# Kernel tuning notes

Hardware: AMD Instinct MI355X
Metric: run time of the kernel (lower is better)

Reference implementation:

```python
import jax, jax.numpy as jnp
import numpy as np

K = 8               # top-k frequencies
PRED_LEN = 96       # prediction_length
LOW_FREQ = 1        # low_frequency cutoff (drops DC)


def setup_inputs() -> dict:
    key = jax.random.key(0)
    x = jax.random.normal(key, (32, 2048, 64), dtype=jnp.float32)
    return {"x": x}


def reference(x):
    b, t, d = x.shape
    x_freq = jnp.fft.rfft(x, axis=1)                 # (b, t//2+1, d) complex
    freqs = jnp.fft.rfftfreq(t).astype(x.dtype)
    if t % 2 == 0:
        x_freq = x_freq[:, LOW_FREQ:-1]              # drop DC and Nyquist
        f = freqs[LOW_FREQ:-1]
    else:
        x_freq = x_freq[:, LOW_FREQ:]
        f = freqs[LOW_FREQ:]

    # top-k over frequency dim (axis=1), independently per (b, d)
    mag = jnp.abs(x_freq)                            # (b, F, d)
    _, idx = jax.lax.top_k(jnp.moveaxis(mag, 1, 2), K)  # (b, d, K), sorted desc
    idx = jnp.moveaxis(idx, 1, 2)                    # (b, K, d)
    x_k = jnp.take_along_axis(x_freq, idx, axis=1)   # (b, K, d) complex
    f_k = f[idx]                                     # (b, K, d)

    # extrapolate: add conjugate (negative) frequencies, then cos-sum
    x2 = jnp.concatenate([x_k, jnp.conj(x_k)], axis=1)  # (b, 2K, d)
    f2 = jnp.concatenate([f_k, -f_k], axis=1)           # (b, 2K, d)
    t_val = jnp.arange(t + PRED_LEN, dtype=x.dtype)     # (T,)
    amp = jnp.abs(x2) / t                               # (b, 2K, d)
    phase = jnp.angle(x2)                               # (b, 2K, d)
    # (b, 2K, T, d) broadcast intermediate, reduced over freq axis
    x_time = amp[:, :, None, :] * jnp.cos(
        2.0 * np.float32(np.pi) * f2[:, :, None, :] * t_val[None, None, :, None]
        + phase[:, :, None, :]
    )
    return x_time.sum(axis=1)                        # (b, t+PRED_LEN, d)
```

## Files before the change

### kernel.cpp

```cpp
#include <hip/hip_runtime.h>
#include <math.h>

#define BB 32
#define TT 2048
#define DD 64
#define PRED 96
#define TP (TT + PRED)
#define KTOP 8
#define NCAND 12
#define NSIG (BB * DD)
#define MARGIN 2e-4f
#define PI_D 3.14159265358979323846

__device__ __forceinline__ int physIdx(int idx) { return idx ^ ((idx >> 5) & 31); }

__device__ __forceinline__ int posOf(int k) {
    return ((k & 7) << 8) | (((k >> 3) & 7) << 5) | (((k >> 6) & 7) << 2) | (k >> 9);
}

__device__ __forceinline__ float2 cadd(float2 a, float2 b) { return make_float2(a.x + b.x, a.y + b.y); }
__device__ __forceinline__ float2 csub(float2 a, float2 b) { return make_float2(a.x - b.x, a.y - b.y); }
__device__ __forceinline__ float2 cmulni(float2 a) { return make_float2(a.y, -a.x); }
__device__ __forceinline__ float2 cmulpi(float2 a) { return make_float2(-a.y, a.x); }
__device__ __forceinline__ float2 cw8(float2 a) {
    const float s = 0.70710678118654752f;
    return make_float2(s * (a.x + a.y), s * (a.y - a.x));
}
__device__ __forceinline__ float2 cw83(float2 a) {
    const float s = 0.70710678118654752f;
    return make_float2(s * (a.y - a.x), -s * (a.x + a.y));
}
__device__ __forceinline__ float2 ctw(float2 a, int m) {
    const float rev = (float)m * (1.0f / 2048.0f);
    const float c = __builtin_amdgcn_cosf(rev);
    const float s = __builtin_amdgcn_sinf(rev);
    return make_float2(a.x * c + a.y * s, a.y * c - a.x * s);
}

__device__ __forceinline__ void radix8(float2* r) {
    float2 E0, E1, E2, E3, O0, O1, O2, O3;
    {
        float2 s0 = cadd(r[0], r[4]), s1 = csub(r[0], r[4]);
        float2 s2 = cadd(r[2], r[6]), s3 = csub(r[2], r[6]);
        E0 = cadd(s0, s2); E2 = csub(s0, s2);
        E1 = cadd(s1, cmulni(s3)); E3 = cadd(s1, cmulpi(s3));
    }
    {
        float2 s0 = cadd(r[1], r[5]), s1 = csub(r[1], r[5]);
        float2 s2 = cadd(r[3], r[7]), s3 = csub(r[3], r[7]);
        O0 = cadd(s0, s2); O2 = csub(s0, s2);
        O1 = cadd(s1, cmulni(s3)); O3 = cadd(s1, cmulpi(s3));
    }
    const float2 w1 = cw8(O1), w2 = cmulni(O2), w3 = cw83(O3);
    r[0] = cadd(E0, O0); r[4] = csub(E0, O0);
    r[1] = cadd(E1, w1); r[5] = csub(E1, w1);
    r[2] = cadd(E2, w2); r[6] = csub(E2, w2);
    r[3] = cadd(E3, w3); r[7] = csub(E3, w3);
}

__global__ __launch_bounds__(256) void fft_topk_kernel(const float* __restrict__ x,
                                                       int* __restrict__ idxw,
                                                       float* __restrict__ rew,
                                                       float* __restrict__ imw) {
    __shared__ float2 Z[TT];
    __shared__ unsigned long long keys[TT];
    __shared__ int    candS[2][NCAND];
    __shared__ int    flagS[2];
    __shared__ double resR[2][NCAND], resI[2][NCAND], resM[2][NCAND];
    __shared__ double2 wA[32];
    __shared__ double2 wB[64];

    const int i    = blockIdx.x;
    const int xcd  = i & 7;
    const int slot = i >> 3;
    const int b    = xcd * 4 + (slot >> 5);
    const int dp   = slot & 31;
    const int t    = threadIdx.x;

    const float2* xv = (const float2*)x;
    const size_t base = (size_t)b * TT * (DD / 2) + dp;
    float2 r[8];
    #pragma unroll
    for (int q = 0; q < 8; ++q) r[q] = xv[base + (size_t)(t + 256 * q) * (DD / 2)];

    radix8(r);
    #pragma unroll
    for (int p = 1; p < 8; ++p) r[p] = ctw(r[p], (p * t) & (TT - 1));
    #pragma unroll
    for (int p = 0; p < 8; ++p) Z[physIdx(t + (p << 8))] = r[p];
    __syncthreads();

    const int S2 = (t >> 5) << 8, j2 = t & 31;
    #pragma unroll
    for (int p = 0; p < 8; ++p) r[p] = Z[physIdx(S2 + j2 + (p << 5))];
    radix8(r);
    #pragma unroll
    for (int p = 1; p < 8; ++p) r[p] = ctw(r[p], (8 * p * j2) & (TT - 1));
    #pragma unroll
    for (int p = 0; p < 8; ++p) Z[physIdx(S2 + j2 + (p << 5))] = r[p];
    __syncthreads();

    const int S3 = (t >> 2) << 5, j3 = t & 3;
    #pragma unroll
    for (int p = 0; p < 8; ++p) r[p] = Z[physIdx(S3 + j3 + (p << 2))];
    radix8(r);
    #pragma unroll
    for (int p = 1; p < 8; ++p) r[p] = ctw(r[p], (64 * p * j3) & (TT - 1));
    #pragma unroll
    for (int p = 0; p < 8; ++p) Z[physIdx(S3 + j3 + (p << 2))] = r[p];
    __syncthreads();

    #pragma unroll
    for (int g = 0; g < 2; ++g) {
        const int b4 = 8 * t + 4 * g;
        const float2 a = Z[physIdx(b4)],     bb = Z[physIdx(b4 + 1)];
        const float2 c = Z[physIdx(b4 + 2)], dd = Z[physIdx(b4 + 3)];
        const float2 s0 = cadd(a, c), s1 = csub(a, c);
        const float2 s2 = cadd(bb, dd), s3 = csub(bb, dd);
        Z[physIdx(b4)]     = cadd(s0, s2);
        Z[physIdx(b4 + 1)] = cadd(s1, cmulni(s3));
        Z[physIdx(b4 + 2)] = csub(s0, s2);
        Z[physIdx(b4 + 3)] = cadd(s1, cmulpi(s3));
    }
    __syncthreads();

    if (t < 2) keys[t * 1024] = 0ULL;
    #pragma unroll
    for (int p = 0; p < 4; ++p) {
        const int k = 4 * t + 1 + p;
        if (k <= TT / 2 - 1) {
            const float2 z = Z[physIdx(posOf(k))];
            const float2 y = Z[physIdx(posOf(TT - k))];
            const float x1r = 0.5f * (z.x + y.x), x1i = 0.5f * (z.y - y.y);
            const float x2r = 0.5f * (z.y + y.y), x2i = 0.5f * (y.x - z.x);
            const float m1 = x1r * x1r + x1i * x1i;
            const float m2 = x2r * x2r + x2i * x2i;
            keys[k]        = ((unsigned long long)__float_as_uint(m1) << 32) | (unsigned)(4095 - k);
            keys[1024 + k] = ((unsigned long long)__float_as_uint(m2) << 32) | (unsigned)(4095 - k);
        }
    }
    __syncthreads();

    const int wv = t >> 6, lane = t & 63;
    if (wv < 2) {
        const int sig = wv;
        unsigned long long kk[16];
        #pragma unroll
        for (int m = 0; m < 16; ++m) kk[m] = keys[sig * 1024 + lane + 64 * m];
        unsigned long long local = 0;
        #pragma unroll
        for (int m = 0; m < 16; ++m) local = (kk[m] > local) ? kk[m] : local;

        unsigned long long mykey = 0;
        for (int pass = 0; pass < NCAND; ++pass) {
            unsigned long long w = local;
            #pragma unroll
            for (int off = 1; off < 64; off <<= 1) {
                const unsigned long long o = __shfl_xor(w, off, 64);
                if (o > w) w = o;
            }
            if (w == local && w != 0ULL) {
                #pragma unroll
                for (int m = 0; m < 16; ++m) if (kk[m] == w) kk[m] = 0ULL;
                local = 0;
                #pragma unroll
                for (int m = 0; m < 16; ++m) local = (kk[m] > local) ? kk[m] : local;
            }
            if (lane == pass) mykey = w;
        }

        const unsigned long long k7 = __shfl(mykey, 7, 64);
        const unsigned long long k8 = __shfl(mykey, 8, 64);
        const float m8 = __uint_as_float((unsigned)(k7 >> 32));
        const float m9 = __uint_as_float((unsigned)(k8 >> 32));
        const int flg = (m8 - m9 <= MARGIN * m8) ? 1 : 0;
        if (lane == 0) flagS[sig] = flg;

        const int kwin = 4095 - (int)(mykey & 0xFFFFFFFFULL);
        if (lane < NCAND) candS[sig][lane] = kwin;
        if (!flg && lane < KTOP) {
            const float2 z = Z[physIdx(posOf(kwin))];
            const float2 y = Z[physIdx(posOf(TT - kwin))];
            float cr, ci;
            if (sig == 0) { cr = 0.5f * (z.x + y.x); ci = 0.5f * (z.y - y.y); }
            else          { cr = 0.5f * (z.y + y.y); ci = 0.5f * (y.x - z.x); }
            const int s_sig = b * DD + 2 * dp + sig;
            idxw[s_sig * KTOP + lane] = kwin;
            rew[s_sig * KTOP + lane]  = cr * (2.0f / (float)TT);
            imw[s_sig * KTOP + lane]  = ci * (2.0f / (float)TT);
        }
    }
    __syncthreads();

    if (flagS[0] | flagS[1]) {
        float2* xs2 = (float2*)keys;
        #pragma unroll
        for (int q = 0; q < 8; ++q)
            xs2[t + 256 * q] = xv[base + (size_t)(t + 256 * q) * (DD / 2)];
        if (t < 32) {
            const double th = -PI_D * (double)t / 16.0;
            wA[t] = make_double2(cos(th), sin(th));
        } else if (t < 96) {
            const int j = t - 32;
            const double th = -2.0 * PI_D * (double)j / (double)TT;
            wB[j] = make_double2(cos(th), sin(th));
        }
        __syncthreads();

        for (int sig = 0; sig < 2; ++sig) {
            if (!flagS[sig]) continue;
            for (int rr = wv; rr < NCAND; rr += 4) {
                const int k = candS[sig][rr];
                double ar = 0.0, ai = 0.0;
                for (int m = 0; m < TT / 64; ++m) {
                    const int n   = lane + 64 * m;
                    const int ix  = (k * n) & (TT - 1);
                    const double2 a  = wA[ix >> 6];
                    const double2 bw = wB[ix & 63];
                    const double wr = a.x * bw.x - a.y * bw.y;
                    const double wi = a.x * bw.y + a.y * bw.x;
                    const double xn = (sig == 0) ? (double)xs2[n].x : (double)xs2[n].y;
                    ar = fma(xn, wr, ar);
                    ai = fma(xn, wi, ai);
                }
                #pragma unroll
                for (int off = 32; off; off >>= 1) {
                    ar += __shfl_xor(ar, off, 64);
                    ai += __shfl_xor(ai, off, 64);
                }
                if (lane == 0) {
                    resR[sig][rr] = ar; resI[sig][rr] = ai;
                    resM[sig][rr] = ar * ar + ai * ai;
                }
            }
        }
        __syncthreads();

        if (t < 2 * NCAND) {
            const int sig = t / NCAND, rr = t % NCAND;
            if (flagS[sig]) {
                const double m = resM[sig][rr];
                const int    k = candS[sig][rr];
                int rank = 0;
                for (int r2 = 0; r2 < NCAND; ++r2) {
                    const double m2 = resM[sig][r2];
                    const int    k2 = candS[sig][r2];
                    if (m2 > m || (m2 == m && k2 < k)) ++rank;
                }
                if (rank < KTOP) {
                    const int s_sig = b * DD + 2 * dp + sig;
                    idxw[s_sig * KTOP + rank] = k;
                    rew[s_sig * KTOP + rank]  = (float)(resR[sig][rr] * (2.0 / (double)TT));
                    imw[s_sig * KTOP + rank]  = (float)(resI[sig][rr] * (2.0 / (double)TT));
                }
            }
        }
    }
}

__global__ __launch_bounds__(256) void synth_kernel(const int* __restrict__ idxw,
                                                    const float* __restrict__ rew,
                                                    const float* __restrict__ imw,
                                                    float* __restrict__ out) {
    const int NT   = (TP + 127) / 128;
    const int b    = blockIdx.x / NT;
    const int tile = blockIdx.x % NT;
    const int tid  = threadIdx.x;
    const int d    = tid & 63;
    const int tq   = tid >> 6;
    const int s    = b * DD + d;

    int   kk[KTOP];
    float rr[KTOP], ii[KTOP];
    int   jj[KTOP];
    #pragma unroll
    for (int p = 0; p < KTOP; ++p) {
        kk[p] = idxw[s * KTOP + p];
        rr[p] = rew[s * KTOP + p];
        ii[p] = imw[s * KTOP + p];
    }
    const int t0 = tile * 128 + tq * 32;
    #pragma unroll
    for (int p = 0; p < KTOP; ++p) jj[p] = (kk[p] * t0) & (TT - 1);

    const float invT = 1.0f / (float)TT;
    for (int i = 0; i < 32; ++i) {
        const int t = t0 + i;
        if (t < TP) {
            float acc = 0.0f;
            #pragma unroll
            for (int p = 0; p < KTOP; ++p) {
                const float rev = (float)jj[p] * invT;
                const float c  = __builtin_amdgcn_cosf(rev);
                const float sn = __builtin_amdgcn_sinf(rev);
                acc += rr[p] * c - ii[p] * sn;
            }
            out[((size_t)b * TP + t) * DD + d] = acc;
        }
        #pragma unroll
        for (int p = 0; p < KTOP; ++p) jj[p] = (jj[p] + kk[p]) & (TT - 1);
    }
}

extern "C" void kernel_launch(void* const* d_in, const int* in_sizes, int n_in,
                              void* d_out, int out_size, void* d_ws, size_t ws_size,
                              hipStream_t stream) {
    const float* x = (const float*)d_in[0];
    float* out = (float*)d_out;

    char* p = (char*)d_ws;
    int*   idxw = (int*)p;     p += (size_t)NSIG * KTOP * sizeof(int);
    float* rew  = (float*)p;   p += (size_t)NSIG * KTOP * sizeof(float);
    float* imw  = (float*)p;

    fft_topk_kernel<<<NSIG / 2, 256, 0, stream>>>(x, idxw, rew, imw);

    const int NT = (TP + 127) / 128;
    synth_kernel<<<BB * NT, 256, 0, stream>>>(idxw, rew, imw, out);
}
```

Before: 113.2 us.

## Pre-transpose input for coalesced FFT loads and drop shared key buffer

Adds a transpose kernel that writes the input into a per-signal contiguous layout in workspace, staged through a padded LDS tile. The FFT kernel then reads each signal with unit stride instead of striding across the channel dimension. It also drops the 16 KB shared keys array: top-k magnitudes are now computed from Z straight into registers, and the fallback path reuses Z as its staging buffer. This buys coalesced loads and lower LDS use, which should help occupancy, at the price of an extra kernel launch and a full extra read and write of the input through global memory.

```diff
diff --git a/kernel.cpp b/kernel.cpp
--- a/kernel.cpp
+++ b/kernel.cpp
@@ -58,12 +58,40 @@
     r[3] = cadd(E3, w3); r[7] = csub(E3, w3);
 }
 
-__global__ __launch_bounds__(256) void fft_topk_kernel(const float* __restrict__ x,
+__global__ __launch_bounds__(256) void transpose_kernel(const float* __restrict__ x,
+                                                        float2* __restrict__ xT) {
+    __shared__ float2 tile[64][33];
+
+    const int i     = blockIdx.x;
+    const int xcd   = i & 7;
+    const int slot  = i >> 3;
+    const int b     = xcd * 4 + (slot >> 5);
+    const int ntile = slot & 31;
+    const int n0    = ntile * 64;
+    const int t     = threadIdx.x;
+
+    const float2* xv = (const float2*)x;
+    const int c = t & 31, r0 = t >> 5;
+    #pragma unroll
+    for (int q = 0; q < 8; ++q) {
+        const int n = n0 + r0 + 8 * q;
+        tile[r0 + 8 * q][c] = xv[((size_t)b * TT + n) * (DD / 2) + c];
+    }
+    __syncthreads();
+
+    const int ln = t & 63, wq = t >> 6;
+    #pragma unroll
+    for (int q = 0; q < 8; ++q) {
+        const int dp = wq + 4 * q;
+        xT[((size_t)(b * (DD / 2) + dp)) * TT + n0 + ln] = tile[ln][dp];
+    }
+}
+
+__global__ __launch_bounds__(256) void fft_topk_kernel(const float2* __restrict__ xT,
                                                        int* __restrict__ idxw,
                                                        float* __restrict__ rew,
                                                        float* __restrict__ imw) {
     __shared__ float2 Z[TT];
-    __shared__ unsigned long long keys[TT];
     __shared__ int    candS[2][NCAND];
     __shared__ int    flagS[2];
     __shared__ double resR[2][NCAND], resI[2][NCAND], resM[2][NCAND];
@@ -77,11 +105,10 @@
     const int dp   = slot & 31;
     const int t    = threadIdx.x;
 
-    const float2* xv = (const float2*)x;
-    const size_t base = (size_t)b * TT * (DD / 2) + dp;
+    const size_t base = (size_t)(b * (DD / 2) + dp) * TT;
     float2 r[8];
     #pragma unroll
-    for (int q = 0; q < 8; ++q) r[q] = xv[base + (size_t)(t + 256 * q) * (DD / 2)];
+    for (int q = 0; q < 8; ++q) r[q] = xT[base + t + 256 * q];
 
     radix8(r);
     #pragma unroll
@@ -124,29 +151,25 @@
     }
     __syncthreads();
 
-    if (t < 2) keys[t * 1024] = 0ULL;
-    #pragma unroll
-    for (int p = 0; p < 4; ++p) {
-        const int k = 4 * t + 1 + p;
-        if (k <= TT / 2 - 1) {
-            const float2 z = Z[physIdx(posOf(k))];
-            const float2 y = Z[physIdx(posOf(TT - k))];
-            const float x1r = 0.5f * (z.x + y.x), x1i = 0.5f * (z.y - y.y);
-            const float x2r = 0.5f * (z.y + y.y), x2i = 0.5f * (y.x - z.x);
-            const float m1 = x1r * x1r + x1i * x1i;
-            const float m2 = x2r * x2r + x2i * x2i;
-            keys[k]        = ((unsigned long long)__float_as_uint(m1) << 32) | (unsigned)(4095 - k);
-            keys[1024 + k] = ((unsigned long long)__float_as_uint(m2) << 32) | (unsigned)(4095 - k);
-        }
-    }
-    __syncthreads();
-
     const int wv = t >> 6, lane = t & 63;
     if (wv < 2) {
         const int sig = wv;
         unsigned long long kk[16];
         #pragma unroll
-        for (int m = 0; m < 16; ++m) kk[m] = keys[sig * 1024 + lane + 64 * m];
+        for (int m = 0; m < 16; ++m) {
+            const int k = lane + 64 * m;
+            unsigned long long key = 0ULL;
+            if (k != 0) {
+                const float2 z = Z[physIdx(posOf(k))];
+                const float2 y = Z[physIdx(posOf(TT - k))];
+                float cr, ci;
+                if (sig == 0) { cr = 0.5f * (z.x + y.x); ci = 0.5f * (z.y - y.y); }
+                else          { cr = 0.5f * (z.y + y.y); ci = 0.5f * (y.x - z.x); }
+                const float mg = cr * cr + ci * ci;
+                key = ((unsigned long long)__float_as_uint(mg) << 32) | (unsigned)(4095 - k);
+            }
+            kk[m] = key;
+        }
         unsigned long long local = 0;
         #pragma unroll
         for (int m = 0; m < 16; ++m) local = (kk[m] > local) ? kk[m] : local;
@@ -193,10 +216,9 @@
     __syncthreads();
 
     if (flagS[0] | flagS[1]) {
-        float2* xs2 = (float2*)keys;
         #pragma unroll
         for (int q = 0; q < 8; ++q)
-            xs2[t + 256 * q] = xv[base + (size_t)(t + 256 * q) * (DD / 2)];
+            Z[t + 256 * q] = xT[base + t + 256 * q];
         if (t < 32) {
             const double th = -PI_D * (double)t / 16.0;
             wA[t] = make_double2(cos(th), sin(th));
@@ -219,7 +241,7 @@
                     const double2 bw = wB[ix & 63];
                     const double wr = a.x * bw.x - a.y * bw.y;
                     const double wi = a.x * bw.y + a.y * bw.x;
-                    const double xn = (sig == 0) ? (double)xs2[n].x : (double)xs2[n].y;
+                    const double xn = (sig == 0) ? (double)Z[n].x : (double)Z[n].y;
                     ar = fma(xn, wr, ar);
                     ai = fma(xn, wi, ai);
                 }
@@ -309,11 +331,13 @@
     float* out = (float*)d_out;
 
     char* p = (char*)d_ws;
+    float2* xT = (float2*)p;   p += (size_t)BB * (DD / 2) * TT * sizeof(float2);
     int*   idxw = (int*)p;     p += (size_t)NSIG * KTOP * sizeof(int);
     float* rew  = (float*)p;   p += (size_t)NSIG * KTOP * sizeof(float);
     float* imw  = (float*)p;
 
-    fft_topk_kernel<<<NSIG / 2, 256, 0, stream>>>(x, idxw, rew, imw);
+    transpose_kernel<<<NSIG / 2, 256, 0, stream>>>(x, xT);
+    fft_topk_kernel<<<NSIG / 2, 256, 0, stream>>>(xT, idxw, rew, imw);
 
     const int NT = (TP + 127) / 128;
     synth_kernel<<<BB * NT, 256, 0, stream>>>(idxw, rew, imw, out);
```

After: 115.3 us. About the same (+1.8%).

## Replace iterative shuffle top-k with register bitonic sort and 32-bit keys

Applied to the files above, without the earlier changes.

Magnitudes are now computed directly into per-lane registers as 32-bit keys, with the mantissa truncated to carry the index in the low 11 bits. The 64-bit shared keys array and its barrier are removed. Top-k selection uses a per-lane 16-element bitonic sort followed by a butterfly merge across lanes, replacing the 12-pass serial max extraction. The key truncation lowers magnitude precision, so NCAND and MARGIN are raised to send more near-ties to the double-precision fallback, which now reuses the Z buffer for staging.

```diff
diff --git a/kernel.cpp b/kernel.cpp
--- a/kernel.cpp
+++ b/kernel.cpp
@@ -7,9 +7,9 @@
 #define PRED 96
 #define TP (TT + PRED)
 #define KTOP 8
-#define NCAND 12
+#define NCAND 16
 #define NSIG (BB * DD)
-#define MARGIN 2e-4f
+#define MARGIN 8e-4f
 #define PI_D 3.14159265358979323846
 
 __device__ __forceinline__ int physIdx(int idx) { return idx ^ ((idx >> 5) & 31); }
@@ -63,7 +63,6 @@
                                                        float* __restrict__ rew,
                                                        float* __restrict__ imw) {
     __shared__ float2 Z[TT];
-    __shared__ unsigned long long keys[TT];
     __shared__ int    candS[2][NCAND];
     __shared__ int    flagS[2];
     __shared__ double resR[2][NCAND], resI[2][NCAND], resM[2][NCAND];
@@ -124,59 +123,80 @@
     }
     __syncthreads();
 
-    if (t < 2) keys[t * 1024] = 0ULL;
-    #pragma unroll
-    for (int p = 0; p < 4; ++p) {
-        const int k = 4 * t + 1 + p;
-        if (k <= TT / 2 - 1) {
-            const float2 z = Z[physIdx(posOf(k))];
-            const float2 y = Z[physIdx(posOf(TT - k))];
-            const float x1r = 0.5f * (z.x + y.x), x1i = 0.5f * (z.y - y.y);
-            const float x2r = 0.5f * (z.y + y.y), x2i = 0.5f * (y.x - z.x);
-            const float m1 = x1r * x1r + x1i * x1i;
-            const float m2 = x2r * x2r + x2i * x2i;
-            keys[k]        = ((unsigned long long)__float_as_uint(m1) << 32) | (unsigned)(4095 - k);
-            keys[1024 + k] = ((unsigned long long)__float_as_uint(m2) << 32) | (unsigned)(4095 - k);
-        }
-    }
-    __syncthreads();
-
     const int wv = t >> 6, lane = t & 63;
     if (wv < 2) {
         const int sig = wv;
-        unsigned long long kk[16];
-        #pragma unroll
-        for (int m = 0; m < 16; ++m) kk[m] = keys[sig * 1024 + lane + 64 * m];
-        unsigned long long local = 0;
-        #pragma unroll
-        for (int m = 0; m < 16; ++m) local = (kk[m] > local) ? kk[m] : local;
-
-        unsigned long long mykey = 0;
-        for (int pass = 0; pass < NCAND; ++pass) {
-            unsigned long long w = local;
-            #pragma unroll
-            for (int off = 1; off < 64; off <<= 1) {
-                const unsigned long long o = __shfl_xor(w, off, 64);
-                if (o > w) w = o;
-            }
-            if (w == local && w != 0ULL) {
+        unsigned A[16];
+        #pragma unroll
+        for (int m = 0; m < 16; ++m) {
+            const int k = lane + (m << 6);
+            unsigned key = 0u;
+            if (k != 0) {
+                const float2 z = Z[physIdx(posOf(k))];
+                const float2 y = Z[physIdx(posOf(TT - k))];
+                float cr, ci;
+                if (sig == 0) { cr = 0.5f * (z.x + y.x); ci = 0.5f * (z.y - y.y); }
+                else          { cr = 0.5f * (z.y + y.y); ci = 0.5f * (y.x - z.x); }
+                const float mg = cr * cr + ci * ci;
+                key = (__float_as_uint(mg) & 0xFFFFF800u) | (unsigned)(2047 - k);
+            }
+            A[m] = key;
+        }
+
+        #pragma unroll
+        for (int sz = 2; sz <= 16; sz <<= 1) {
+            #pragma unroll
+            for (int d = sz >> 1; d > 0; d >>= 1) {
                 #pragma unroll
-                for (int m = 0; m < 16; ++m) if (kk[m] == w) kk[m] = 0ULL;
-                local = 0;
+                for (int i2 = 0; i2 < 16; ++i2) {
+                    const int j2i = i2 ^ d;
+                    if (j2i > i2) {
+                        const bool desc = ((i2 & sz) == 0);
+                        const unsigned a = A[i2], b2 = A[j2i];
+                        const unsigned mx = a > b2 ? a : b2;
+                        const unsigned mn = a > b2 ? b2 : a;
+                        A[i2]  = desc ? mx : mn;
+                        A[j2i] = desc ? mn : mx;
+                    }
+                }
+            }
+        }
+
+        #pragma unroll
+        for (int off = 1; off < 64; off <<= 1) {
+            unsigned Bv[16];
+            #pragma unroll
+            for (int i2 = 0; i2 < 16; ++i2)
+                Bv[i2] = (unsigned)__shfl_xor((int)A[i2], off, 64);
+            #pragma unroll
+            for (int i2 = 0; i2 < 16; ++i2) {
+                const unsigned o = Bv[15 - i2];
+                A[i2] = A[i2] > o ? A[i2] : o;
+            }
+            #pragma unroll
+            for (int d = 8; d > 0; d >>= 1) {
                 #pragma unroll
-                for (int m = 0; m < 16; ++m) local = (kk[m] > local) ? kk[m] : local;
-            }
-            if (lane == pass) mykey = w;
-        }
-
-        const unsigned long long k7 = __shfl(mykey, 7, 64);
-        const unsigned long long k8 = __shfl(mykey, 8, 64);
-        const float m8 = __uint_as_float((unsigned)(k7 >> 32));
-        const float m9 = __uint_as_float((unsigned)(k8 >> 32));
-        const int flg = (m8 - m9 <= MARGIN * m8) ? 1 : 0;
+                for (int i2 = 0; i2 < 16; ++i2) {
+                    if ((i2 & d) == 0) {
+                        const int j2i = i2 + d;
+                        const unsigned a = A[i2], b2 = A[j2i];
+                        A[i2]  = a > b2 ? a : b2;
+                        A[j2i] = a > b2 ? b2 : a;
+                    }
+                }
+            }
+        }
+
+        const float mf8 = __uint_as_float(A[7] & 0xFFFFF800u);
+        const float mf9 = __uint_as_float(A[8] & 0xFFFFF800u);
+        const int flg = (mf8 - mf9 <= MARGIN * mf8) ? 1 : 0;
         if (lane == 0) flagS[sig] = flg;
 
-        const int kwin = 4095 - (int)(mykey & 0xFFFFFFFFULL);
+        unsigned myk = 0u;
+        #pragma unroll
+        for (int i2 = 0; i2 < 16; ++i2) myk = (lane == i2) ? A[i2] : myk;
+        const int kwin = 2047 - (int)(myk & 0x7FFu);
+
         if (lane < NCAND) candS[sig][lane] = kwin;
         if (!flg && lane < KTOP) {
             const float2 z = Z[physIdx(posOf(kwin))];
@@ -193,10 +213,9 @@
     __syncthreads();
 
     if (flagS[0] | flagS[1]) {
-        float2* xs2 = (float2*)keys;
         #pragma unroll
         for (int q = 0; q < 8; ++q)
-            xs2[t + 256 * q] = xv[base + (size_t)(t + 256 * q) * (DD / 2)];
+            Z[t + 256 * q] = xv[base + (size_t)(t + 256 * q) * (DD / 2)];
         if (t < 32) {
             const double th = -PI_D * (double)t / 16.0;
             wA[t] = make_double2(cos(th), sin(th));
@@ -219,7 +238,7 @@
                     const double2 bw = wB[ix & 63];
                     const double wr = a.x * bw.x - a.y * bw.y;
                     const double wi = a.x * bw.y + a.y * bw.x;
-                    const double xn = (sig == 0) ? (double)xs2[n].x : (double)xs2[n].y;
+                    const double xn = (sig == 0) ? (double)Z[n].x : (double)Z[n].y;
                     ar = fma(xn, wr, ar);
                     ai = fma(xn, wi, ai);
                 }
```

Result: no change. 113.0 us (-0.2%).
